# Performance work log

Hardware: AMD Instinct MI355X
Metric: run time of the kernel (lower is better)

The kernel has to match this reference:

```python
import jax, jax.numpy as jnp
import numpy as np

N_NODES = 100000
N_EDGES = 1600000
NUM_FEATURES = 64
HIDDEN = 256
NUM_CLASSES = 47
ORDER = 8
DROPNODE_RATE = 0.5


def setup_inputs() -> dict:
    key = jax.random.key(0)
    ks = jax.random.split(key, 8)
    X = jax.random.normal(ks[0], (N_NODES, NUM_FEATURES), dtype=jnp.float32)
    src = jax.random.randint(ks[1], (N_EDGES,), 0, N_NODES, dtype=jnp.int64)
    dst = jax.random.randint(ks[2], (N_EDGES,), 0, N_NODES, dtype=jnp.int64)
    edge_w = jax.random.uniform(ks[3], (N_EDGES,), dtype=jnp.float32)
    W0 = jax.random.normal(ks[4], (NUM_FEATURES, HIDDEN), dtype=jnp.float32) * (1.0 / np.sqrt(NUM_FEATURES))
    b0 = jnp.zeros((HIDDEN,), dtype=jnp.float32)
    W1 = jax.random.normal(ks[5], (HIDDEN, NUM_CLASSES), dtype=jnp.float32) * (1.0 / np.sqrt(HIDDEN))
    b1 = jnp.zeros((NUM_CLASSES,), dtype=jnp.float32)
    return {"X": X, "src": src, "dst": dst, "edge_w": edge_w,
            "W0": W0, "b0": b0, "W1": W1, "b1": b1}


def _normalize(e):
    # embedding / (1e-12 + ||embedding||_2 along last dim)
    return e / (1e-12 + jnp.linalg.norm(e, axis=-1, keepdims=True))


def reference(X, src, dst, edge_w, W0, b0, W1, b1):
    n = X.shape[0]
    # rand_prop (eval mode): scale by keep prob, then `order` rounds of
    # edge-weighted SpMM: x <- scatter_sum(x[src] * w_e, dst)
    x = X * (1.0 - DROPNODE_RATE)
    prop = x
    for _ in range(ORDER):
        msg = x[src] * edge_w[:, None]          # [E, F] u_mul_e
        x = jax.ops.segment_sum(msg, dst, num_segments=n)  # sum reduce at dst
        prop = prop + x
    Xp = jax.lax.stop_gradient(prop / (ORDER + 1.0))  # .detach_()
    # node_norm=True, use_bn=False; eval -> dropout is identity
    Xp = _normalize(Xp)
    h = Xp @ W0 + b0
    h = jax.nn.relu(h)
    h = _normalize(h)
    out = h @ W1 + b1
    return out
```

## Files before the change

kernel.cpp:

```cpp
#include <hip/hip_runtime.h>
#include <hip/hip_fp16.h>
#include <math.h>

#define N_NODES 100000
#define N_EDGES 1600000
#define NF 64
#define ORDER 8
#define NBLK 391
#define MAX_ADJ (N_EDGES + 8 * N_NODES)

struct __align__(8) H4 { __half2 a, b; };

using f16x8 = __attribute__((ext_vector_type(8))) _Float16;
using f32x4 = __attribute__((ext_vector_type(4))) float;


__global__ __launch_bounds__(256) void zero_ints(int* __restrict__ c, int n) {
  int i = blockIdx.x * 256 + threadIdx.x;
  if (i < n) c[i] = 0;
}

__global__ __launch_bounds__(256) void hist_kernel(const int* __restrict__ dst,
                                                   int* __restrict__ counts) {
  int e = blockIdx.x * 256 + threadIdx.x;
  if (e < N_EDGES) atomicAdd(&counts[dst[e]], 1);
}

__device__ __forceinline__ int padc(int c) { return (c + 7) & ~7; }

__global__ __launch_bounds__(256) void reduce_counts(const int* __restrict__ counts,
                                                     int* __restrict__ blockSums) {
  int i = blockIdx.x * 256 + threadIdx.x;
  int v = (i < N_NODES) ? padc(counts[i]) : 0;
  #pragma unroll
  for (int m = 1; m < 64; m <<= 1) v += __shfl_xor(v, m, 64);
  __shared__ int s[4];
  if ((threadIdx.x & 63) == 0) s[threadIdx.x >> 6] = v;
  __syncthreads();
  if (threadIdx.x == 0) blockSums[blockIdx.x] = s[0] + s[1] + s[2] + s[3];
}

__global__ __launch_bounds__(512) void scan_partials(const int* __restrict__ blockSums,
                                                     int* __restrict__ blockOffs) {
  __shared__ int s[512];
  int t = threadIdx.x;
  int v = (t < NBLK) ? blockSums[t] : 0;
  s[t] = v;
  __syncthreads();
  for (int off = 1; off < 512; off <<= 1) {
    int u = (t >= off) ? s[t - off] : 0;
    __syncthreads();
    s[t] += u;
    __syncthreads();
  }
  if (t < NBLK) blockOffs[t] = s[t] - v;
}

__global__ __launch_bounds__(256) void scan_blocks(const int* __restrict__ counts,
    const int* __restrict__ blockOffs, int* __restrict__ row_start,
    int* __restrict__ cursor) {
  __shared__ int s[256];
  int t = threadIdx.x;
  int i = blockIdx.x * 256 + t;
  int v = (i < N_NODES) ? padc(counts[i]) : 0;
  s[t] = v;
  __syncthreads();
  for (int off = 1; off < 256; off <<= 1) {
    int u = (t >= off) ? s[t - off] : 0;
    __syncthreads();
    s[t] += u;
    __syncthreads();
  }
  int excl = s[t] - v + blockOffs[blockIdx.x];
  if (i < N_NODES) { row_start[i] = excl; cursor[i] = excl; }
  if (i == N_NODES - 1) row_start[N_NODES] = excl + v;
}

__global__ __launch_bounds__(256) void fill_kernel(const int* __restrict__ src,
    const int* __restrict__ dst, const float* __restrict__ ew,
    int* __restrict__ cursor, unsigned int* __restrict__ adj) {
  int e = blockIdx.x * 256 + threadIdx.x;
  if (e >= N_EDGES) return;
  int d = dst[e];
  int pos = atomicAdd(&cursor[d], 1);
  unsigned int w15 = (unsigned int)rintf(ew[e] * 32767.0f);
  adj[pos] = ((unsigned int)src[e] << 15) | w15;
}

__global__ __launch_bounds__(256) void pack_weights(const float* __restrict__ W0,
    const float* __restrict__ W1, _Float16* __restrict__ W0Th,
    _Float16* __restrict__ W1Th) {
  int t = threadIdx.x;
  for (int k = 0; k < 64; ++k)
    W0Th[t * 64 + k] = (_Float16)W0[k * 256 + t];
  for (int c = 0; c < 48; ++c) {
    float v = (c < 47) ? W1[t * 47 + c] : 0.0f;
    W1Th[c * 256 + t] = (_Float16)v;
  }
}


__global__ __launch_bounds__(256) void init_kernel(const float4* __restrict__ X,
    H4* __restrict__ xc, float4* __restrict__ prop, int n4) {
  int i = blockIdx.x * 256 + threadIdx.x;
  if (i >= n4) return;
  float4 v = X[i];
  v.x *= 0.5f; v.y *= 0.5f; v.z *= 0.5f; v.w *= 0.5f;
  prop[i] = v;
  H4 h;
  h.a = __floats2half2_rn(v.x, v.y);
  h.b = __floats2half2_rn(v.z, v.w);
  xc[i] = h;
}

template<bool ACC>
__global__ __launch_bounds__(256) void spmm_csr(const __half2* __restrict__ x,
    const int* __restrict__ row_start, const unsigned int* __restrict__ adj,
    __half2* __restrict__ xn, float2* __restrict__ prop) {
  const int node = blockIdx.x * 8 + (threadIdx.x >> 5);
  const int f2 = threadIdx.x & 31;
  const int beg = row_start[node];
  const int nb = (row_start[node + 1] - beg) >> 3;
  const size_t o = (size_t)node * 32 + f2;
  float2 xin;
  if (ACC) xin = __half22float2(x[o]);
  float2 a0 = make_float2(0.f, 0.f), a1 = a0;

  unsigned int e[8];
  __half2 v[8];
  if (nb > 0) {
    #pragma unroll
    for (int j = 0; j < 8; ++j) e[j] = adj[beg + j];
    #pragma unroll
    for (int j = 0; j < 8; ++j) v[j] = x[(size_t)(e[j] >> 15) * 32 + f2];
  }
  for (int b = 1; b < nb; ++b) {
    const int q = beg + 8 * b;
    unsigned int ne[8];
    __half2 nv[8];
    #pragma unroll
    for (int j = 0; j < 8; ++j) ne[j] = adj[q + j];
    #pragma unroll
    for (int j = 0; j < 8; ++j) nv[j] = x[(size_t)(ne[j] >> 15) * 32 + f2];
    #pragma unroll
    for (int j = 0; j < 8; ++j) {
      float w = (float)(e[j] & 0x7fffu) * (1.0f / 32767.0f);
      float2 f = __half22float2(v[j]);
      if (j & 1) { a1.x = fmaf(f.x, w, a1.x); a1.y = fmaf(f.y, w, a1.y); }
      else       { a0.x = fmaf(f.x, w, a0.x); a0.y = fmaf(f.y, w, a0.y); }
    }
    #pragma unroll
    for (int j = 0; j < 8; ++j) { e[j] = ne[j]; v[j] = nv[j]; }
  }
  if (nb > 0) {
    #pragma unroll
    for (int j = 0; j < 8; ++j) {
      float w = (float)(e[j] & 0x7fffu) * (1.0f / 32767.0f);
      float2 f = __half22float2(v[j]);
      if (j & 1) { a1.x = fmaf(f.x, w, a1.x); a1.y = fmaf(f.y, w, a1.y); }
      else       { a0.x = fmaf(f.x, w, a0.x); a0.y = fmaf(f.y, w, a0.y); }
    }
  }
  a0.x += a1.x; a0.y += a1.y;
  xn[o] = __floats2half2_rn(a0.x, a0.y);
  if (ACC) {
    float2 pr = prop[o];
    pr.x += xin.x + a0.x;
    pr.y += xin.y + a0.y;
    prop[o] = pr;
  }
}

__global__ __launch_bounds__(256) void tail_kernel(
    const float* __restrict__ prop, const float* __restrict__ b0,
    const _Float16* __restrict__ W0Th, const _Float16* __restrict__ W1Th,
    const float* __restrict__ b1, float* __restrict__ out) {
  __shared__ __align__(16) _Float16 sXp[32][72];
  __shared__ __align__(16) _Float16 sH[32][264];
  __shared__ float sPart[32][8];
  __shared__ float sHinv[32];

  const int t = threadIdx.x;
  const int lane = t & 63;
  const int w = t >> 6;
  const int l15 = lane & 15;
  const int l4 = lane >> 4;
  const int base = blockIdx.x * 32;

  #pragma unroll
  for (int it = 0; it < 8; ++it) {
    const int nb = it * 4 + w;
    float v = prop[(size_t)(base + nb) * NF + lane];
    float ss = v * v;
    #pragma unroll
    for (int m = 1; m < 64; m <<= 1) ss += __shfl_xor(ss, m, 64);
    float nrm = sqrtf(ss) * (1.0f / 9.0f);
    float scale = (1.0f / 9.0f) / (1e-12f + nrm);
    sXp[nb][lane] = (_Float16)(v * scale);
  }
  __syncthreads();

  f32x4 acc1[2][4];
  #pragma unroll
  for (int j = 0; j < 4; ++j) {
    float bv = b0[(w * 4 + j) * 16 + l15];
    #pragma unroll
    for (int mt = 0; mt < 2; ++mt)
      acc1[mt][j] = (f32x4){bv, bv, bv, bv};
  }
  #pragma unroll
  for (int ks = 0; ks < 2; ++ks) {
    const int koff = l4 * 8 + ks * 32;
    f16x8 a0 = *(const f16x8*)&sXp[l15][koff];
    f16x8 a1 = *(const f16x8*)&sXp[16 + l15][koff];
    #pragma unroll
    for (int j = 0; j < 4; ++j) {
      f16x8 b = *(const f16x8*)&W0Th[(size_t)((w * 4 + j) * 16 + l15) * 64 + koff];
      acc1[0][j] = __builtin_amdgcn_mfma_f32_16x16x32_f16(a0, b, acc1[0][j], 0, 0, 0);
      acc1[1][j] = __builtin_amdgcn_mfma_f32_16x16x32_f16(a1, b, acc1[1][j], 0, 0, 0);
    }
  }

  #pragma unroll
  for (int mt = 0; mt < 2; ++mt) {
    #pragma unroll
    for (int r = 0; r < 4; ++r) {
      float s = 0.0f;
      #pragma unroll
      for (int j = 0; j < 4; ++j) {
        float x = fmaxf(acc1[mt][j][r], 0.0f);
        acc1[mt][j][r] = x;
        s = fmaf(x, x, s);
      }
      #pragma unroll
      for (int m = 1; m < 16; m <<= 1) s += __shfl_xor(s, m, 64);
      if (l15 == 0) sPart[mt * 16 + l4 * 4 + r][w] = s;
    }
  }
  __syncthreads();

  if (t < 32) {
    float s = sPart[t][0] + sPart[t][1] + sPart[t][2] + sPart[t][3];
    sHinv[t] = 1.0f / (1e-12f + sqrtf(s));
  }
  __syncthreads();

  #pragma unroll
  for (int mt = 0; mt < 2; ++mt) {
    #pragma unroll
    for (int r = 0; r < 4; ++r) {
      const int row = mt * 16 + l4 * 4 + r;
      const float sc = sHinv[row];
      #pragma unroll
      for (int j = 0; j < 4; ++j)
        sH[row][(w * 4 + j) * 16 + l15] = (_Float16)(acc1[mt][j][r] * sc);
    }
  }
  __syncthreads();

  if (w < 3) {
    const int c = w * 16 + l15;
    float bv = (c < 47) ? b1[c] : 0.0f;
    f32x4 acc2[2];
    acc2[0] = (f32x4){bv, bv, bv, bv};
    acc2[1] = (f32x4){bv, bv, bv, bv};
    #pragma unroll
    for (int ks = 0; ks < 8; ++ks) {
      const int koff = l4 * 8 + ks * 32;
      f16x8 b = *(const f16x8*)&W1Th[(size_t)(w * 16 + l15) * 256 + koff];
      f16x8 a0 = *(const f16x8*)&sH[l15][koff];
      f16x8 a1 = *(const f16x8*)&sH[16 + l15][koff];
      acc2[0] = __builtin_amdgcn_mfma_f32_16x16x32_f16(a0, b, acc2[0], 0, 0, 0);
      acc2[1] = __builtin_amdgcn_mfma_f32_16x16x32_f16(a1, b, acc2[1], 0, 0, 0);
    }
    if (c < 47) {
      #pragma unroll
      for (int mt = 0; mt < 2; ++mt) {
        #pragma unroll
        for (int r = 0; r < 4; ++r) {
          const int node = base + mt * 16 + l4 * 4 + r;
          out[(size_t)node * 47 + c] = acc2[mt][r];
        }
      }
    }
  }
}

extern "C" void kernel_launch(void* const* d_in, const int* in_sizes, int n_in,
                              void* d_out, int out_size, void* d_ws, size_t ws_size,
                              hipStream_t stream) {
  (void)in_sizes; (void)n_in; (void)out_size; (void)ws_size;
  const float* X   = (const float*)d_in[0];
  const int*   src = (const int*)d_in[1];
  const int*   dst = (const int*)d_in[2];
  const float* ew  = (const float*)d_in[3];
  const float* W0  = (const float*)d_in[4];
  const float* b0  = (const float*)d_in[5];
  const float* W1  = (const float*)d_in[6];
  const float* b1  = (const float*)d_in[7];
  float* out = (float*)d_out;

  const size_t nf = (size_t)N_NODES * NF;
  __half* bufA = (__half*)d_ws;
  __half* bufB = bufA + nf;
  float*  prop = (float*)(bufB + nf);
  int* counts     = (int*)(prop + nf);
  int* row_start  = counts + N_NODES;
  int* cursor     = row_start + (N_NODES + 1);
  int* blockSums  = cursor + N_NODES;
  int* blockOffs  = blockSums + NBLK;
  _Float16* W0Th  = (_Float16*)(((uintptr_t)(blockOffs + NBLK) + 15) & ~(uintptr_t)15);
  _Float16* W1Th  = W0Th + 256 * 64;
  unsigned int* adj = (unsigned int*)(((uintptr_t)(W1Th + 48 * 256) + 15) & ~(uintptr_t)15);

  const int eblocks = (N_EDGES + 255) / 256;

  zero_ints<<<NBLK, 256, 0, stream>>>(counts, N_NODES);
  hipMemsetAsync(adj, 0, (size_t)MAX_ADJ * 4, stream);
  hist_kernel<<<eblocks, 256, 0, stream>>>(dst, counts);
  reduce_counts<<<NBLK, 256, 0, stream>>>(counts, blockSums);
  scan_partials<<<1, 512, 0, stream>>>(blockSums, blockOffs);
  scan_blocks<<<NBLK, 256, 0, stream>>>(counts, blockOffs, row_start, cursor);
  fill_kernel<<<eblocks, 256, 0, stream>>>(src, dst, ew, cursor, adj);
  pack_weights<<<1, 256, 0, stream>>>(W0, W1, W0Th, W1Th);

  const int n4 = (int)(nf / 4);
  init_kernel<<<(n4 + 255) / 256, 256, 0, stream>>>(
      (const float4*)X, (H4*)bufA, (float4*)prop, n4);

  __half* xc = bufA;
  __half* xn = bufB;
  for (int r = 0; r < ORDER; ++r) {
    if (r & 1) {
      spmm_csr<true><<<N_NODES / 8, 256, 0, stream>>>(
          (const __half2*)xc, row_start, adj, (__half2*)xn, (float2*)prop);
    } else {
      spmm_csr<false><<<N_NODES / 8, 256, 0, stream>>>(
          (const __half2*)xc, row_start, adj, (__half2*)xn, (float2*)prop);
    }
    __half* tmp = xc; xc = xn; xn = tmp;
  }

  tail_kernel<<<N_NODES / 32, 256, 0, stream>>>(prop, b0, W0Th, W1Th, b1, out);
}
```

Before: 505.1 us.

## Deepen SpMM gather prefetch to two batches and partition CSR fill by destination range

```diff
diff --git a/kernel.cpp b/kernel.cpp
--- a/kernel.cpp
+++ b/kernel.cpp
@@ -8,6 +8,7 @@
 #define ORDER 8
 #define NBLK 391
 #define MAX_ADJ (N_EDGES + 8 * N_NODES)
+#define NPR (N_NODES / 8)
 
 struct __align__(8) H4 { __half2 a, b; };
 
@@ -79,9 +80,11 @@
 __global__ __launch_bounds__(256) void fill_kernel(const int* __restrict__ src,
     const int* __restrict__ dst, const float* __restrict__ ew,
     int* __restrict__ cursor, unsigned int* __restrict__ adj) {
-  int e = blockIdx.x * 256 + threadIdx.x;
+  const int rg = blockIdx.x & 7;
+  const int e = (blockIdx.x >> 3) * 256 + threadIdx.x;
   if (e >= N_EDGES) return;
   int d = dst[e];
+  if ((unsigned)(d - rg * NPR) >= (unsigned)NPR) return;
   int pos = atomicAdd(&cursor[d], 1);
   unsigned int w15 = (unsigned int)rintf(ew[e] * 32767.0f);
   adj[pos] = ((unsigned int)src[e] << 15) | w15;
@@ -126,39 +129,36 @@
   if (ACC) xin = __half22float2(x[o]);
   float2 a0 = make_float2(0.f, 0.f), a1 = a0;
 
-  unsigned int e[8];
-  __half2 v[8];
+  unsigned int e0[8] = {0}, e1[8] = {0};
+  __half2 v0[8], v1[8];
   if (nb > 0) {
     #pragma unroll
-    for (int j = 0; j < 8; ++j) e[j] = adj[beg + j];
-    #pragma unroll
-    for (int j = 0; j < 8; ++j) v[j] = x[(size_t)(e[j] >> 15) * 32 + f2];
-  }
-  for (int b = 1; b < nb; ++b) {
-    const int q = beg + 8 * b;
-    unsigned int ne[8];
-    __half2 nv[8];
-    #pragma unroll
-    for (int j = 0; j < 8; ++j) ne[j] = adj[q + j];
-    #pragma unroll
-    for (int j = 0; j < 8; ++j) nv[j] = x[(size_t)(ne[j] >> 15) * 32 + f2];
+    for (int j = 0; j < 8; ++j) e0[j] = adj[beg + j];
+    #pragma unroll
+    for (int j = 0; j < 8; ++j) v0[j] = x[(size_t)(e0[j] >> 15) * 32 + f2];
+  }
+  if (nb > 1) {
+    #pragma unroll
+    for (int j = 0; j < 8; ++j) e1[j] = adj[beg + 8 + j];
+    #pragma unroll
+    for (int j = 0; j < 8; ++j) v1[j] = x[(size_t)(e1[j] >> 15) * 32 + f2];
+  }
+  for (int b = 0; b < nb; ++b) {
     #pragma unroll
     for (int j = 0; j < 8; ++j) {
-      float w = (float)(e[j] & 0x7fffu) * (1.0f / 32767.0f);
-      float2 f = __half22float2(v[j]);
+      float w = (float)(e0[j] & 0x7fffu) * (1.0f / 32767.0f);
+      float2 f = __half22float2(v0[j]);
       if (j & 1) { a1.x = fmaf(f.x, w, a1.x); a1.y = fmaf(f.y, w, a1.y); }
       else       { a0.x = fmaf(f.x, w, a0.x); a0.y = fmaf(f.y, w, a0.y); }
     }
     #pragma unroll
-    for (int j = 0; j < 8; ++j) { e[j] = ne[j]; v[j] = nv[j]; }
-  }
-  if (nb > 0) {
-    #pragma unroll
-    for (int j = 0; j < 8; ++j) {
-      float w = (float)(e[j] & 0x7fffu) * (1.0f / 32767.0f);
-      float2 f = __half22float2(v[j]);
-      if (j & 1) { a1.x = fmaf(f.x, w, a1.x); a1.y = fmaf(f.y, w, a1.y); }
-      else       { a0.x = fmaf(f.x, w, a0.x); a0.y = fmaf(f.y, w, a0.y); }
+    for (int j = 0; j < 8; ++j) { e0[j] = e1[j]; v0[j] = v1[j]; }
+    if (b + 2 < nb) {
+      const int q = beg + 8 * (b + 2);
+      #pragma unroll
+      for (int j = 0; j < 8; ++j) e1[j] = adj[q + j];
+      #pragma unroll
+      for (int j = 0; j < 8; ++j) v1[j] = x[(size_t)(e1[j] >> 15) * 32 + f2];
     }
   }
   a0.x += a1.x; a0.y += a1.y;
@@ -321,7 +321,7 @@
   reduce_counts<<<NBLK, 256, 0, stream>>>(counts, blockSums);
   scan_partials<<<1, 512, 0, stream>>>(blockSums, blockOffs);
   scan_blocks<<<NBLK, 256, 0, stream>>>(counts, blockOffs, row_start, cursor);
-  fill_kernel<<<eblocks, 256, 0, stream>>>(src, dst, ew, cursor, adj);
+  fill_kernel<<<8 * eblocks, 256, 0, stream>>>(src, dst, ew, cursor, adj);
   pack_weights<<<1, 256, 0, stream>>>(W0, W1, W0Th, W1Th);
 
   const int n4 = (int)(nf / 4);
```

Measured after the change: 484.2 us. 4.1% less time.
